# Kernel optimization log

Hardware: AMD Instinct MI355X
Metric: run time of the kernel (lower is better)

Reference implementation:

```python
import jax, jax.numpy as jnp
import numpy as np

B, S, E, H, V, C = 1024, 64, 256, 512, 128, 32


def setup_inputs() -> dict:
    key = jax.random.key(0)
    ks = jax.random.split(key, 12)
    s = 0.05
    emb_table = jax.random.normal(ks[0], (V, E), jnp.float32) * s
    emb_table = emb_table.at[0].set(0.0)  # padding_idx = 0
    return {
        "x_in": jax.random.randint(ks[1], (B, S), 0, V),
        "x_lens": jax.random.randint(ks[2], (B,), 1, S + 1),
        "emb_table": emb_table,
        "W_ih": jax.random.normal(ks[3], (H, E), jnp.float32) * s,
        "b_ih": jnp.zeros((H,), jnp.float32),
        "W_hh": jax.random.normal(ks[4], (H, H), jnp.float32) * s,
        "b_hh": jnp.zeros((H,), jnp.float32),
        "W1": jax.random.normal(ks[5], (H, H), jnp.float32) * s,
        "b1": jnp.zeros((H,), jnp.float32),
        "W2": jax.random.normal(ks[6], (C, H), jnp.float32) * s,
        "b2": jnp.zeros((C,), jnp.float32),
    }


def reference(x_in, x_lens, emb_table, W_ih, b_ih, W_hh, b_hh, W1, b1, W2, b2):
    # Embedding lookup: [B, S, E]
    x_emb = emb_table[x_in]

    # Elman RNN: h_t = tanh(x_t W_ih^T + b_ih + h_{t-1} W_hh^T + b_hh)
    def step(h, x_t):
        h = jnp.tanh(x_t @ W_ih.T + b_ih + h @ W_hh.T + b_hh)
        return h, h

    h0 = jnp.zeros((x_in.shape[0], W_hh.shape[0]), x_emb.dtype)
    _, ys = jax.lax.scan(step, h0, jnp.swapaxes(x_emb, 0, 1))  # ys: [S, B, H]
    y_out = jnp.swapaxes(ys, 0, 1)  # [B, S, H]

    # column_gather: pick hidden state at position x_lens-1 for each row
    last = y_out[jnp.arange(y_out.shape[0]), x_lens - 1]  # [B, H]

    # MLP head (dropout is identity in eval mode)
    hidden = jax.nn.relu(last @ W1.T + b1)
    logits = hidden @ W2.T + b2  # [B, C]
    return logits
```

## Files before the change

### kernel.cpp

```cpp
#include <hip/hip_runtime.h>
#include <hip/hip_bf16.h>

#define BB 1024
#define SS 64
#define EE 256
#define HH 512
#define VV 128
#define CC 32

typedef _Float16 f16;
typedef _Float16 f16x4 __attribute__((ext_vector_type(4)));
typedef _Float16 f16x8 __attribute__((ext_vector_type(8)));
typedef float    f32x4 __attribute__((ext_vector_type(4)));

#define CVT_TOT4   (65536 + 65536 + 4096)
#define CVT_STRIDE (96 * 256)

__global__ __launch_bounds__(256) void prep_kernel(
    const float* __restrict__ emb, const float* __restrict__ W_ih,
    const float* __restrict__ b_ih, const float* __restrict__ b_hh,
    const float* __restrict__ W_hh, const float* __restrict__ W1,
    const float* __restrict__ W2,
    f16* __restrict__ P, f16* __restrict__ Whf,
    f16* __restrict__ W1f, f16* __restrict__ W2f)
{
    if (blockIdx.x < VV) {
        __shared__ float er[EE];
        const int v = blockIdx.x;
        for (int i = threadIdx.x; i < EE; i += 256) er[i] = emb[(size_t)v * EE + i];
        __syncthreads();
        for (int h = threadIdx.x; h < HH; h += 256) {
            const float4* wr = (const float4*)(W_ih + (size_t)h * EE);
            float s = 0.f;
            #pragma unroll 4
            for (int e4 = 0; e4 < EE / 4; ++e4) {
                float4 w = wr[e4];
                const float* e = er + e4 * 4;
                s += w.x * e[0] + w.y * e[1] + w.z * e[2] + w.w * e[3];
            }
            P[(size_t)v * HH + h] = (f16)(s + b_ih[h] + b_hh[h]);
        }
    } else {
        for (int i = (blockIdx.x - VV) * 256 + threadIdx.x; i < CVT_TOT4;
             i += CVT_STRIDE) {
            const float* src; f16* dst; int j;
            if (i < 65536)       { src = W_hh; dst = Whf; j = i; }
            else if (i < 131072) { src = W1;   dst = W1f; j = i - 65536; }
            else                 { src = W2;   dst = W2f; j = i - 131072; }
            float4 x = ((const float4*)src)[j];
            f16x4 y;
            y[0] = (f16)x.x; y[1] = (f16)x.y; y[2] = (f16)x.z; y[3] = (f16)x.w;
            *(f16x4*)(dst + (size_t)j * 4) = y;
        }
    }
}

#define KSREG 12
#define KSLDS 4
#define HSTR  520

#define KB(t,k) "v"(bfr[t][k])
#define KBT(t)  KB(t,0), KB(t,1), KB(t,2), KB(t,3), KB(t,4), KB(t,5), \
                KB(t,6), KB(t,7), KB(t,8), KB(t,9), KB(t,10), KB(t,11)

__global__
__attribute__((amdgpu_flat_work_group_size(512, 512)))
__attribute__((amdgpu_waves_per_eu(2, 2)))
void rnn_fused(
    const int* __restrict__ x_in, const int* __restrict__ x_lens,
    const f16* __restrict__ Whf, const f16* __restrict__ P,
    const f16* __restrict__ W1f, const float* __restrict__ b1,
    const f16* __restrict__ W2f, const float* __restrict__ b2,
    float* __restrict__ out)
{
    __shared__ __align__(16) f16 hbuf[16 * HSTR];
    __shared__ __align__(16) f16 wlds[8 * 4 * KSLDS * 64 * 8];
    __shared__ int xin[16 * SS];
    __shared__ int lens[16];

    const int tid  = threadIdx.x;
    const int r0   = blockIdx.x * 16;
    const int wave = tid >> 6;
    const int lane = tid & 63;
    const int lrow = lane & 15;
    const int quad = lane >> 4;
    const int n0w  = wave * 64;

    f16x8 bfr[4][KSREG];
    #pragma unroll
    for (int t = 0; t < 4; ++t) {
        const f16* wr = Whf + (size_t)(n0w + 16 * t + lrow) * HH + quad * 8;
        #pragma unroll
        for (int ks = 0; ks < KSREG; ++ks)
            bfr[t][ks] = *(const f16x8*)(wr + ks * 32);
        #pragma unroll
        for (int ks = 0; ks < KSLDS; ++ks)
            *(f16x8*)(wlds + ((((wave * 4 + t) * KSLDS + ks) * 64 + lane) << 3)) =
                *(const f16x8*)(wr + (KSREG + ks) * 32);
    }

    for (int i = tid; i < 16 * (SS / 4); i += 512)
        ((int4*)xin)[i] = ((const int4*)(x_in + (size_t)r0 * SS))[i];
    if (tid < 16) lens[tid] = x_lens[r0 + tid];
    __syncthreads();

    const int   mylen = lens[lrow];
    const f16*  arow  = hbuf + lrow * HSTR + quad * 8;
    f16*        hwr   = hbuf + lrow * HSTR + n0w + quad * 4;
    const f16*  pbase = P + n0w + quad * 4;

    f16x4 lastreg[4];

    for (int st = 0; st < SS; ++st) {
        asm volatile("" :: KBT(0), KBT(1), KBT(2), KBT(3));

        f32x4 acc0 = {0,0,0,0}, acc1 = {0,0,0,0}, acc2 = {0,0,0,0}, acc3 = {0,0,0,0};
        if (st) {
            #pragma unroll
            for (int ks = 0; ks < KSREG; ++ks) {
                f16x8 a = *(const f16x8*)(arow + ks * 32);
                acc0 = __builtin_amdgcn_mfma_f32_16x16x32_f16(bfr[0][ks], a, acc0, 0, 0, 0);
                acc1 = __builtin_amdgcn_mfma_f32_16x16x32_f16(bfr[1][ks], a, acc1, 0, 0, 0);
                acc2 = __builtin_amdgcn_mfma_f32_16x16x32_f16(bfr[2][ks], a, acc2, 0, 0, 0);
                acc3 = __builtin_amdgcn_mfma_f32_16x16x32_f16(bfr[3][ks], a, acc3, 0, 0, 0);
            }
            #pragma unroll
            for (int ks = 0; ks < KSLDS; ++ks) {
                f16x8 a  = *(const f16x8*)(arow + (KSREG + ks) * 32);
                f16x8 b0 = *(const f16x8*)(wlds + ((((wave * 4 + 0) * KSLDS + ks) * 64 + lane) << 3));
                f16x8 b1 = *(const f16x8*)(wlds + ((((wave * 4 + 1) * KSLDS + ks) * 64 + lane) << 3));
                f16x8 b2 = *(const f16x8*)(wlds + ((((wave * 4 + 2) * KSLDS + ks) * 64 + lane) << 3));
                f16x8 b3 = *(const f16x8*)(wlds + ((((wave * 4 + 3) * KSLDS + ks) * 64 + lane) << 3));
                acc0 = __builtin_amdgcn_mfma_f32_16x16x32_f16(b0, a, acc0, 0, 0, 0);
                acc1 = __builtin_amdgcn_mfma_f32_16x16x32_f16(b1, a, acc1, 0, 0, 0);
                acc2 = __builtin_amdgcn_mfma_f32_16x16x32_f16(b2, a, acc2, 0, 0, 0);
                acc3 = __builtin_amdgcn_mfma_f32_16x16x32_f16(b3, a, acc3, 0, 0, 0);
            }
        }

        const int  tok = xin[lrow * SS + st];
        const f16* pb  = pbase + (size_t)tok * HH;
        f16x4 pv0 = *(const f16x4*)(pb);
        f16x4 pv1 = *(const f16x4*)(pb + 16);
        f16x4 pv2 = *(const f16x4*)(pb + 32);
        f16x4 pv3 = *(const f16x4*)(pb + 48);

        __syncthreads();

        const int tp1 = st + 1;
        const bool wr_last = (mylen == tp1);
        #pragma unroll
        for (int t = 0; t < 4; ++t) {
            const f32x4 acc = (t == 0) ? acc0 : (t == 1) ? acc1 : (t == 2) ? acc2 : acc3;
            const f16x4 pv  = (t == 0) ? pv0  : (t == 1) ? pv1  : (t == 2) ? pv2  : pv3;
            f16x4 hv;
            #pragma unroll
            for (int r = 0; r < 4; ++r) {
                float z = acc[r] + (float)pv[r];
                float e = __expf(2.f * z);
                hv[r] = (f16)(1.f - 2.f / (e + 1.f));
            }
            *(f16x4*)(hwr + 16 * t) = hv;
            if (wr_last) lastreg[t] = hv;
        }

        __syncthreads();
    }

    #pragma unroll
    for (int t = 0; t < 4; ++t)
        *(f16x4*)(hwr + 16 * t) = lastreg[t];
    __syncthreads();

    f16* hid = wlds;
    {
        f32x4 acc0 = {0,0,0,0}, acc1 = {0,0,0,0}, acc2 = {0,0,0,0}, acc3 = {0,0,0,0};
        #pragma unroll 4
        for (int ks = 0; ks < 16; ++ks) {
            f16x8 a  = *(const f16x8*)(arow + ks * 32);
            const f16* w1r = W1f + (size_t)(n0w + lrow) * HH + ks * 32 + quad * 8;
            f16x8 b0 = *(const f16x8*)(w1r);
            f16x8 b1 = *(const f16x8*)(w1r + 16 * HH);
            f16x8 b2 = *(const f16x8*)(w1r + 32 * HH);
            f16x8 b3 = *(const f16x8*)(w1r + 48 * HH);
            acc0 = __builtin_amdgcn_mfma_f32_16x16x32_f16(b0, a, acc0, 0, 0, 0);
            acc1 = __builtin_amdgcn_mfma_f32_16x16x32_f16(b1, a, acc1, 0, 0, 0);
            acc2 = __builtin_amdgcn_mfma_f32_16x16x32_f16(b2, a, acc2, 0, 0, 0);
            acc3 = __builtin_amdgcn_mfma_f32_16x16x32_f16(b3, a, acc3, 0, 0, 0);
        }
        __syncthreads();
        f16* hwr2 = hid + lrow * HSTR + n0w + quad * 4;
        #pragma unroll
        for (int t = 0; t < 4; ++t) {
            const f32x4 acc = (t == 0) ? acc0 : (t == 1) ? acc1 : (t == 2) ? acc2 : acc3;
            const float4 bv = *(const float4*)(b1 + n0w + 16 * t + quad * 4);
            const float  bb[4] = {bv.x, bv.y, bv.z, bv.w};
            f16x4 hv;
            #pragma unroll
            for (int r = 0; r < 4; ++r)
                hv[r] = (f16)fmaxf(acc[r] + bb[r], 0.f);
            *(f16x4*)(hwr2 + 16 * t) = hv;
        }
    }
    __syncthreads();

    if (wave < 2) {
        const f16* harow = hid + lrow * HSTR + quad * 8;
        f32x4 acc = {0,0,0,0};
        #pragma unroll 4
        for (int ks = 0; ks < 16; ++ks) {
            f16x8 a = *(const f16x8*)(harow + ks * 32);
            f16x8 b = *(const f16x8*)(W2f + (size_t)(wave * 16 + lrow) * HH
                                      + ks * 32 + quad * 8);
            acc = __builtin_amdgcn_mfma_f32_16x16x32_f16(b, a, acc, 0, 0, 0);
        }
        const float4 bv = *(const float4*)(b2 + wave * 16 + quad * 4);
        float4 o;
        o.x = acc[0] + bv.x; o.y = acc[1] + bv.y;
        o.z = acc[2] + bv.z; o.w = acc[3] + bv.w;
        *(float4*)(out + (size_t)(r0 + lrow) * CC + wave * 16 + quad * 4) = o;
    }
}

extern "C" void kernel_launch(void* const* d_in, const int* in_sizes, int n_in,
                              void* d_out, int out_size, void* d_ws, size_t ws_size,
                              hipStream_t stream)
{
    const int*   x_in   = (const int*)d_in[0];
    const int*   x_lens = (const int*)d_in[1];
    const float* emb    = (const float*)d_in[2];
    const float* W_ih   = (const float*)d_in[3];
    const float* b_ih   = (const float*)d_in[4];
    const float* W_hh   = (const float*)d_in[5];
    const float* b_hh   = (const float*)d_in[6];
    const float* W1     = (const float*)d_in[7];
    const float* b1     = (const float*)d_in[8];
    const float* W2     = (const float*)d_in[9];
    const float* b2     = (const float*)d_in[10];
    float* out = (float*)d_out;

    char* ws = (char*)d_ws;
    f16* P   = (f16*)ws;
    f16* Whf = (f16*)(ws + (256 << 10));
    f16* W1f = (f16*)(ws + (256 << 10) + (512 << 10));
    f16* W2f = (f16*)(ws + (256 << 10) + (1 << 20));

    hipLaunchKernelGGL(prep_kernel, dim3(VV + 96), dim3(256), 0, stream,
                       emb, W_ih, b_ih, b_hh, W_hh, W1, W2, P, Whf, W1f, W2f);
    hipLaunchKernelGGL(rnn_fused, dim3(BB / 16), dim3(512), 0, stream,
                       x_in, x_lens, Whf, P, W1f, b1, W2f, b2, out);
}
```

Before: 278.0 us.

## Double-buffer hidden state to drop a barrier per step, swizzle LDS, enlarge weight LDS

The hidden-state buffer becomes double-buffered so each recurrence step needs one block barrier instead of two. The padded row stride is replaced with an XOR swizzle to avoid LDS bank conflicts. Nearly all of the register-excess W_hh slice moves into a larger LDS region, and one fragment stays in an extra register. Token ids are read straight from global memory each step, and the final hidden state is written to a global scratch buffer, then reloaded. This adds global traffic and a larger LDS footprint in exchange for fewer synchronisations.

New measurement: 278.0 us. No clear change (+0.0%).

```diff
diff --git a/kernel.cpp b/kernel.cpp
--- a/kernel.cpp
+++ b/kernel.cpp
@@ -57,7 +57,6 @@
 
 #define KSREG 12
 #define KSLDS 4
-#define HSTR  520
 
 #define KB(t,k) "v"(bfr[t][k])
 #define KBT(t)  KB(t,0), KB(t,1), KB(t,2), KB(t,3), KB(t,4), KB(t,5), \
@@ -71,12 +70,13 @@
     const f16* __restrict__ Whf, const f16* __restrict__ P,
     const f16* __restrict__ W1f, const float* __restrict__ b1,
     const f16* __restrict__ W2f, const float* __restrict__ b2,
-    float* __restrict__ out)
+    f16* __restrict__ last, float* __restrict__ out)
 {
-    __shared__ __align__(16) f16 hbuf[16 * HSTR];
-    __shared__ __align__(16) f16 wlds[8 * 4 * KSLDS * 64 * 8];
-    __shared__ int xin[16 * SS];
-    __shared__ int lens[16];
+    __shared__ __align__(16) f16 hbuf[2 * 16 * 512];
+    __shared__ __align__(16) f16 wlds[61440];
+
+    char* hb = (char*)hbuf;
+    char* wl = (char*)wlds;
 
     const int tid  = threadIdx.x;
     const int r0   = blockIdx.x * 16;
@@ -86,7 +86,14 @@
     const int quad = lane >> 4;
     const int n0w  = wave * 64;
 
+    const int sw45 = (lrow & 3) << 4;
+    const int sw6  = (lrow & 4) << 4;
+    const int swf  = sw45 | sw6;
+    const int abase = (lrow << 10) + ((quad << 4) ^ sw45);
+    const int wbase = (lrow << 10) + (n0w << 1) + (quad << 3);
+
     f16x8 bfr[4][KSREG];
+    f16x8 bfrX;
     #pragma unroll
     for (int t = 0; t < 4; ++t) {
         const f16* wr = Whf + (size_t)(n0w + 16 * t + lrow) * HH + quad * 8;
@@ -94,31 +101,34 @@
         for (int ks = 0; ks < KSREG; ++ks)
             bfr[t][ks] = *(const f16x8*)(wr + ks * 32);
         #pragma unroll
-        for (int ks = 0; ks < KSLDS; ++ks)
-            *(f16x8*)(wlds + ((((wave * 4 + t) * KSLDS + ks) * 64 + lane) << 3)) =
-                *(const f16x8*)(wr + (KSREG + ks) * 32);
-    }
-
-    for (int i = tid; i < 16 * (SS / 4); i += 512)
-        ((int4*)xin)[i] = ((const int4*)(x_in + (size_t)r0 * SS))[i];
-    if (tid < 16) lens[tid] = x_lens[r0 + tid];
+        for (int ks = 0; ks < KSLDS; ++ks) {
+            f16x8 v = *(const f16x8*)(wr + (KSREG + ks) * 32);
+            if (t == 3 && ks == KSLDS - 1) bfrX = v;
+            else *(f16x8*)(wl + (((wave * 15 + t * 4 + ks) << 10) + (lane << 4))) = v;
+        }
+    }
+
+    const int mylen = x_lens[r0 + lrow];
+    const int xrow  = (r0 + lrow) * SS;
+    const f16* pbase = P + n0w + quad * 4;
+    f16* lastg = last + (size_t)(r0 + lrow) * HH + n0w + quad * 4;
+
     __syncthreads();
 
-    const int   mylen = lens[lrow];
-    const f16*  arow  = hbuf + lrow * HSTR + quad * 8;
-    f16*        hwr   = hbuf + lrow * HSTR + n0w + quad * 4;
-    const f16*  pbase = P + n0w + quad * 4;
-
-    f16x4 lastreg[4];
-
     for (int st = 0; st < SS; ++st) {
-        asm volatile("" :: KBT(0), KBT(1), KBT(2), KBT(3));
+        const int selr = (st & 1) << 14;
+        const int selw = ((st + 1) & 1) << 14;
+
+        const int tok = x_in[xrow + st];
+
+        asm volatile("" :: KBT(0), KBT(1), KBT(2), KBT(3), "v"(bfrX));
 
         f32x4 acc0 = {0,0,0,0}, acc1 = {0,0,0,0}, acc2 = {0,0,0,0}, acc3 = {0,0,0,0};
         if (st) {
+            const int ab = abase + selr;
             #pragma unroll
             for (int ks = 0; ks < KSREG; ++ks) {
-                f16x8 a = *(const f16x8*)(arow + ks * 32);
+                f16x8 a = *(const f16x8*)(hb + ((ab + (ks << 6)) ^ sw6));
                 acc0 = __builtin_amdgcn_mfma_f32_16x16x32_f16(bfr[0][ks], a, acc0, 0, 0, 0);
                 acc1 = __builtin_amdgcn_mfma_f32_16x16x32_f16(bfr[1][ks], a, acc1, 0, 0, 0);
                 acc2 = __builtin_amdgcn_mfma_f32_16x16x32_f16(bfr[2][ks], a, acc2, 0, 0, 0);
@@ -126,29 +136,27 @@
             }
             #pragma unroll
             for (int ks = 0; ks < KSLDS; ++ks) {
-                f16x8 a  = *(const f16x8*)(arow + (KSREG + ks) * 32);
-                f16x8 b0 = *(const f16x8*)(wlds + ((((wave * 4 + 0) * KSLDS + ks) * 64 + lane) << 3));
-                f16x8 b1 = *(const f16x8*)(wlds + ((((wave * 4 + 1) * KSLDS + ks) * 64 + lane) << 3));
-                f16x8 b2 = *(const f16x8*)(wlds + ((((wave * 4 + 2) * KSLDS + ks) * 64 + lane) << 3));
-                f16x8 b3 = *(const f16x8*)(wlds + ((((wave * 4 + 3) * KSLDS + ks) * 64 + lane) << 3));
-                acc0 = __builtin_amdgcn_mfma_f32_16x16x32_f16(b0, a, acc0, 0, 0, 0);
-                acc1 = __builtin_amdgcn_mfma_f32_16x16x32_f16(b1, a, acc1, 0, 0, 0);
-                acc2 = __builtin_amdgcn_mfma_f32_16x16x32_f16(b2, a, acc2, 0, 0, 0);
-                acc3 = __builtin_amdgcn_mfma_f32_16x16x32_f16(b3, a, acc3, 0, 0, 0);
-            }
-        }
-
-        const int  tok = xin[lrow * SS + st];
-        const f16* pb  = pbase + (size_t)tok * HH;
+                f16x8 a  = *(const f16x8*)(hb + ((ab + ((KSREG + ks) << 6)) ^ sw6));
+                f16x8 b0 = *(const f16x8*)(wl + (((wave * 15 +  0 + ks) << 10) + (lane << 4)));
+                f16x8 b1v = *(const f16x8*)(wl + (((wave * 15 +  4 + ks) << 10) + (lane << 4)));
+                f16x8 b2v = *(const f16x8*)(wl + (((wave * 15 +  8 + ks) << 10) + (lane << 4)));
+                f16x8 b3v = (ks == KSLDS - 1) ? bfrX
+                          : *(const f16x8*)(wl + (((wave * 15 + 12 + ks) << 10) + (lane << 4)));
+                acc0 = __builtin_amdgcn_mfma_f32_16x16x32_f16(b0,  a, acc0, 0, 0, 0);
+                acc1 = __builtin_amdgcn_mfma_f32_16x16x32_f16(b1v, a, acc1, 0, 0, 0);
+                acc2 = __builtin_amdgcn_mfma_f32_16x16x32_f16(b2v, a, acc2, 0, 0, 0);
+                acc3 = __builtin_amdgcn_mfma_f32_16x16x32_f16(b3v, a, acc3, 0, 0, 0);
+            }
+        }
+
+        const f16* pb = pbase + (size_t)tok * HH;
         f16x4 pv0 = *(const f16x4*)(pb);
         f16x4 pv1 = *(const f16x4*)(pb + 16);
         f16x4 pv2 = *(const f16x4*)(pb + 32);
         f16x4 pv3 = *(const f16x4*)(pb + 48);
 
-        __syncthreads();
-
-        const int tp1 = st + 1;
-        const bool wr_last = (mylen == tp1);
+        const int wb = wbase + selw;
+        const bool wr_last = (mylen == st + 1);
         #pragma unroll
         for (int t = 0; t < 4; ++t) {
             const f32x4 acc = (t == 0) ? acc0 : (t == 1) ? acc1 : (t == 2) ? acc2 : acc3;
@@ -160,36 +168,37 @@
                 float e = __expf(2.f * z);
                 hv[r] = (f16)(1.f - 2.f / (e + 1.f));
             }
-            *(f16x4*)(hwr + 16 * t) = hv;
-            if (wr_last) lastreg[t] = hv;
+            *(f16x4*)(hb + ((wb + (t << 5)) ^ swf)) = hv;
+            if (wr_last) *(f16x4*)(lastg + 16 * t) = hv;
         }
 
         __syncthreads();
     }
 
-    #pragma unroll
-    for (int t = 0; t < 4; ++t)
-        *(f16x4*)(hwr + 16 * t) = lastreg[t];
+    for (int i = tid; i < 1024; i += 512) {
+        const int row = i >> 6, c = i & 63;
+        const int ofs = (((row << 10) + (c << 4)) ^ ((row & 7) << 4));
+        *(f16x8*)(hb + ofs) =
+            *(const f16x8*)(last + (size_t)(r0 + row) * HH + c * 8);
+    }
     __syncthreads();
 
-    f16* hid = wlds;
     {
         f32x4 acc0 = {0,0,0,0}, acc1 = {0,0,0,0}, acc2 = {0,0,0,0}, acc3 = {0,0,0,0};
         #pragma unroll 4
         for (int ks = 0; ks < 16; ++ks) {
-            f16x8 a  = *(const f16x8*)(arow + ks * 32);
+            f16x8 a = *(const f16x8*)(hb + ((abase + (ks << 6)) ^ sw6));
             const f16* w1r = W1f + (size_t)(n0w + lrow) * HH + ks * 32 + quad * 8;
             f16x8 b0 = *(const f16x8*)(w1r);
-            f16x8 b1 = *(const f16x8*)(w1r + 16 * HH);
-            f16x8 b2 = *(const f16x8*)(w1r + 32 * HH);
-            f16x8 b3 = *(const f16x8*)(w1r + 48 * HH);
-            acc0 = __builtin_amdgcn_mfma_f32_16x16x32_f16(b0, a, acc0, 0, 0, 0);
-            acc1 = __builtin_amdgcn_mfma_f32_16x16x32_f16(b1, a, acc1, 0, 0, 0);
-            acc2 = __builtin_amdgcn_mfma_f32_16x16x32_f16(b2, a, acc2, 0, 0, 0);
-            acc3 = __builtin_amdgcn_mfma_f32_16x16x32_f16(b3, a, acc3, 0, 0, 0);
-        }
-        __syncthreads();
-        f16* hwr2 = hid + lrow * HSTR + n0w + quad * 4;
+            f16x8 b1v = *(const f16x8*)(w1r + 16 * HH);
+            f16x8 b2v = *(const f16x8*)(w1r + 32 * HH);
+            f16x8 b3v = *(const f16x8*)(w1r + 48 * HH);
+            acc0 = __builtin_amdgcn_mfma_f32_16x16x32_f16(b0,  a, acc0, 0, 0, 0);
+            acc1 = __builtin_amdgcn_mfma_f32_16x16x32_f16(b1v, a, acc1, 0, 0, 0);
+            acc2 = __builtin_amdgcn_mfma_f32_16x16x32_f16(b2v, a, acc2, 0, 0, 0);
+            acc3 = __builtin_amdgcn_mfma_f32_16x16x32_f16(b3v, a, acc3, 0, 0, 0);
+        }
+        const int wb = wbase + 16384;
         #pragma unroll
         for (int t = 0; t < 4; ++t) {
             const f32x4 acc = (t == 0) ? acc0 : (t == 1) ? acc1 : (t == 2) ? acc2 : acc3;
@@ -199,17 +208,16 @@
             #pragma unroll
             for (int r = 0; r < 4; ++r)
                 hv[r] = (f16)fmaxf(acc[r] + bb[r], 0.f);
-            *(f16x4*)(hwr2 + 16 * t) = hv;
+            *(f16x4*)(hb + ((wb + (t << 5)) ^ swf)) = hv;
         }
     }
     __syncthreads();
 
     if (wave < 2) {
-        const f16* harow = hid + lrow * HSTR + quad * 8;
         f32x4 acc = {0,0,0,0};
         #pragma unroll 4
         for (int ks = 0; ks < 16; ++ks) {
-            f16x8 a = *(const f16x8*)(harow + ks * 32);
+            f16x8 a = *(const f16x8*)(hb + ((abase + 16384 + (ks << 6)) ^ sw6));
             f16x8 b = *(const f16x8*)(W2f + (size_t)(wave * 16 + lrow) * HH
                                       + ks * 32 + quad * 8);
             acc = __builtin_amdgcn_mfma_f32_16x16x32_f16(b, a, acc, 0, 0, 0);
@@ -240,13 +248,14 @@
     float* out = (float*)d_out;
 
     char* ws = (char*)d_ws;
-    f16* P   = (f16*)ws;
-    f16* Whf = (f16*)(ws + (256 << 10));
-    f16* W1f = (f16*)(ws + (256 << 10) + (512 << 10));
-    f16* W2f = (f16*)(ws + (256 << 10) + (1 << 20));
+    f16* P    = (f16*)ws;
+    f16* Whf  = (f16*)(ws + (128 << 10));
+    f16* W1f  = (f16*)(ws + (640 << 10));
+    f16* W2f  = (f16*)(ws + (1152 << 10));
+    f16* last = (f16*)(ws + (1184 << 10));
 
     hipLaunchKernelGGL(prep_kernel, dim3(VV + 96), dim3(256), 0, stream,
                        emb, W_ih, b_ih, b_hh, W_hh, W1, W2, P, Whf, W1f, W2f);
     hipLaunchKernelGGL(rnn_fused, dim3(BB / 16), dim3(512), 0, stream,
-                       x_in, x_lens, Whf, P, W1f, b1, W2f, b2, out);
+                       x_in, x_lens, Whf, P, W1f, b1, W2f, b2, last, out);
 }
```
